# Kernel tuning notes

Measured on AMD Instinct MI355X. Metric: run time of the kernel, lower is better.

The kernel has to match this reference:

```python
import jax, jax.numpy as jnp
import numpy as np

B, S, D, H = 2, 2048, 1024, 16
DK = D // H

def setup_inputs() -> dict:
    key = jax.random.key(0)
    ks = jax.random.split(key, 12)
    s = 1.0 / np.sqrt(D)
    return {
        "q": jax.random.normal(ks[0], (B, S, D), jnp.float32),
        "k": jax.random.normal(ks[1], (B, S, D), jnp.float32),
        "v": jax.random.normal(ks[2], (B, S, D), jnp.float32),
        "mask": jnp.ones((1, 1, S, S), jnp.int32),
        "Wq": jax.random.normal(ks[3], (D, D), jnp.float32) * s,
        "bq": jnp.zeros((D,), jnp.float32),
        "Wk": jax.random.normal(ks[4], (D, D), jnp.float32) * s,
        "bk": jnp.zeros((D,), jnp.float32),
        "Wv": jax.random.normal(ks[5], (D, D), jnp.float32) * s,
        "bv": jnp.zeros((D,), jnp.float32),
        "Wo": jax.random.normal(ks[6], (D, D), jnp.float32) * s,
        "bo": jnp.zeros((D,), jnp.float32),
    }

def reference(q, k, v, mask, Wq, bq, Wk, bk, Wv, bv, Wo, bo):
    # projections (torch Linear: x @ W^T + b)
    Q = q @ Wq.T + bq
    K = k @ Wk.T + bk
    V = v @ Wv.T + bv
    # split heads: [B,S,D] -> [B,H,S,DK]
    def split(x):
        return x.reshape(B, S, H, DK).transpose(0, 2, 1, 3)
    Qh, Kh, Vh = split(Q), split(K), split(V)
    scores = jnp.einsum('bhqd,bhkd->bhqk', Qh, Kh) / jnp.sqrt(jnp.float32(DK))
    scores = jnp.where(mask == 0, jnp.float32(-1e9), scores)
    attn = jax.nn.softmax(scores, axis=-1)  # dropout p=0.0 -> identity
    x = jnp.einsum('bhqk,bhkd->bhqd', attn, Vh)
    x = x.transpose(0, 2, 1, 3).reshape(B, S, D)
    return x @ Wo.T + bo
```

## Files before the change

kernel.cpp:

```cpp
#include <hip/hip_runtime.h>
#include <hip/hip_bf16.h>
#include <stdint.h>

#define B_    2
#define S_    2048
#define D_    1024
#define H_    16
#define NTOK  (B_ * S_)

typedef __attribute__((ext_vector_type(8))) short bf16x8;
typedef __attribute__((ext_vector_type(4))) float f32x4;
typedef __attribute__((ext_vector_type(2))) float float2v;
typedef __attribute__((ext_vector_type(2))) __bf16 bfv2;

static __device__ __forceinline__ unsigned short f2bf(float f) {
    unsigned int u = __float_as_uint(f);
    unsigned int r = (u + 0x7FFFu + ((u >> 16) & 1u)) >> 16;
    return (unsigned short)r;
}
static __device__ __forceinline__ unsigned int pkbf(float a, float b) {
    float2v fv = {a, b};
    bfv2 r = __builtin_convertvector(fv, bfv2);
    unsigned int u;
    __builtin_memcpy(&u, &r, 4);
    return u;
}

using g_cu32 = __attribute__((address_space(1))) const unsigned int;
using l_u32  = __attribute__((address_space(3))) unsigned int;
static __device__ __forceinline__ void gld16(const void* g, void* l) {
    __builtin_amdgcn_global_load_lds((g_cu32*)g, (l_u32*)l, 16, 0, 0);
}

#define QN ((size_t)NTOK * D_)
#define WN ((size_t)D_ * D_)

__global__ __launch_bounds__(256) void prep_kernel(
    const float* __restrict__ q, const float* __restrict__ k, const float* __restrict__ v,
    const float* __restrict__ Wq, const float* __restrict__ Wk,
    const float* __restrict__ Wv, const float* __restrict__ Wo,
    const int* __restrict__ mask,
    unsigned short* __restrict__ qb, unsigned short* __restrict__ kb,
    unsigned short* __restrict__ vb, unsigned short* __restrict__ wqb,
    unsigned short* __restrict__ wkb, unsigned short* __restrict__ wvb,
    unsigned short* __restrict__ wob, int* __restrict__ flags) {
    __shared__ int anyz;
    if (blockIdx.x < 8192) {
        size_t i = ((size_t)blockIdx.x * 256 + threadIdx.x) * 8;
        const float* s; unsigned short* d; size_t off;
        if (i < QN)          { s = q; d = qb; off = i; }
        else if (i < 2 * QN) { s = k; d = kb; off = i - QN; }
        else if (i < 3 * QN) { s = v; d = vb; off = i - 2 * QN; }
        else {
            size_t j = i - 3 * QN;
            int wi = (int)(j >> 20);
            s = (wi == 0) ? Wq : (wi == 1) ? Wk : (wi == 2) ? Wv : Wo;
            d = (wi == 0) ? wqb : (wi == 1) ? wkb : (wi == 2) ? wvb : wob;
            off = j & (WN - 1);
        }
        float4 a = *(const float4*)(s + off);
        float4 b = *(const float4*)(s + off + 4);
        uint4 pk;
        pk.x = pkbf(a.x, a.y); pk.y = pkbf(a.z, a.w);
        pk.z = pkbf(b.x, b.y); pk.w = pkbf(b.z, b.w);
        *(uint4*)(d + off) = pk;
    } else {
        if (threadIdx.x == 0) anyz = 0;
        __syncthreads();
        int bid2 = blockIdx.x - 8192;
        const int qt = bid2 >> 5, kt = bid2 & 31;
        int az = 0;
        for (int i = threadIdx.x; i < 64 * 64; i += 256) {
            int r = i >> 6, c = i & 63;
            az |= (mask[(size_t)(qt * 64 + r) * S_ + kt * 64 + c] == 0) ? 1 : 0;
        }
        if (az) atomicOr(&anyz, 1);
        __syncthreads();
        if (threadIdx.x == 0) flags[qt * 32 + kt] = anyz;
    }
}

struct GemmArgs {
    const unsigned short* A[3];
    const unsigned short* W[3];
    const float* bias[3];
    void* C[3];
    int mode[3];
    float scale[3];
};

template<int BMT>
__global__ __launch_bounds__(256, 3) void gemm_async(GemmArgs ga) {
    constexpr int AG = BMT / 16;
    constexpr int MI = BMT / 32;
    const int z = blockIdx.z;
    const unsigned short* __restrict__ A = ga.A[z];
    const unsigned short* __restrict__ W = ga.W[z];
    const float* __restrict__ bias = ga.bias[z];
    void* C = ga.C[z];
    const int mode = ga.mode[z];
    const float scl = ga.scale[z];

    __shared__ unsigned short As[AG * 512];
    __shared__ unsigned short Bs[8 * 512];

    const int t    = threadIdx.x;
    const int lane = t & 63;
    const int w    = t >> 6;
    const int fr   = lane & 15;
    const int kq   = lane >> 4;
    const int wrow = w >> 1, wcol = w & 1;
    const int m0 = blockIdx.x * BMT, n0 = blockIdx.y * 128;

    const int sc = lane >> 4;
    const int sr = lane & 15;

    const unsigned short* ga0;
    const unsigned short* ga1 = nullptr;
    unsigned short* la0;
    unsigned short* la1 = nullptr;
    if constexpr (BMT == 128) {
        ga0 = A + (size_t)(m0 + (2 * w) * 16 + sr) * D_ + sc * 8;
        ga1 = ga0 + 16 * D_;
        la0 = &As[(2 * w) * 512];
        la1 = &As[(2 * w + 1) * 512];
    } else {
        ga0 = A + (size_t)(m0 + w * 16 + sr) * D_ + sc * 8;
        la0 = &As[w * 512];
    }
    const unsigned short* gw0 = W + (size_t)(n0 + (2 * w) * 16 + sr) * D_ + sc * 8;
    const unsigned short* gw1 = gw0 + 16 * D_;
    unsigned short* lw0 = &Bs[(2 * w) * 512];
    unsigned short* lw1 = &Bs[(2 * w + 1) * 512];

    int aOff[MI], bOff[4];
#pragma unroll
    for (int mi = 0; mi < MI; ++mi) aOff[mi] = (wrow * MI + mi) * 512 + (kq * 16 + fr) * 8;
#pragma unroll
    for (int ni = 0; ni < 4; ++ni) bOff[ni] = (wcol * 4 + ni) * 512 + (kq * 16 + fr) * 8;

    f32x4 acc[MI][4];
#pragma unroll
    for (int i = 0; i < MI; ++i)
#pragma unroll
        for (int j = 0; j < 4; ++j) acc[i][j] = (f32x4)0.0f;

    for (int k0 = 0; k0 < D_ / 32; ++k0) {
        gld16(ga0, la0);
        if constexpr (BMT == 128) gld16(ga1, la1);
        gld16(gw0, lw0);
        gld16(gw1, lw1);
        ga0 += 32; gw0 += 32; gw1 += 32;
        if constexpr (BMT == 128) ga1 += 32;
        __syncthreads();

        bf16x8 af[MI], bfr[4];
#pragma unroll
        for (int mi = 0; mi < MI; ++mi) af[mi] = *(const bf16x8*)&As[aOff[mi]];
#pragma unroll
        for (int ni = 0; ni < 4; ++ni) bfr[ni] = *(const bf16x8*)&Bs[bOff[ni]];
#pragma unroll
        for (int mi = 0; mi < MI; ++mi)
#pragma unroll
            for (int ni = 0; ni < 4; ++ni)
                acc[mi][ni] = __builtin_amdgcn_mfma_f32_16x16x32_bf16(
                    af[mi], bfr[ni], acc[mi][ni], 0, 0, 0);
        __syncthreads();
    }

    if (mode == 0) {
        float* Co = (float*)C;
#pragma unroll
        for (int ni = 0; ni < 4; ++ni) {
            int col = n0 + wcol * 64 + ni * 16 + fr;
            float bv = bias[col];
#pragma unroll
            for (int mi = 0; mi < MI; ++mi)
#pragma unroll
                for (int r = 0; r < 4; ++r) {
                    int row = m0 + wrow * (BMT / 2) + mi * 16 + kq * 4 + r;
                    Co[(size_t)row * D_ + col] = (acc[mi][ni][r] + bv) * scl;
                }
        }
    } else if (mode == 1) {
        unsigned short* Co = (unsigned short*)C;
#pragma unroll
        for (int ni = 0; ni < 4; ++ni) {
            int col = n0 + wcol * 64 + ni * 16 + fr;
            float bv = bias[col];
#pragma unroll
            for (int mi = 0; mi < MI; ++mi)
#pragma unroll
                for (int r = 0; r < 4; ++r) {
                    int row = m0 + wrow * (BMT / 2) + mi * 16 + kq * 4 + r;
                    Co[(size_t)row * D_ + col] = f2bf((acc[mi][ni][r] + bv) * scl);
                }
        }
    } else {
        unsigned short* Co = (unsigned short*)C;
#pragma unroll
        for (int ni = 0; ni < 4; ++ni) {
            int col = n0 + wcol * 64 + ni * 16 + fr;
            float bv = bias[col];
            int hh = col >> 6, d = col & 63;
#pragma unroll
            for (int mi = 0; mi < MI; ++mi) {
                int tok = m0 + wrow * (BMT / 2) + mi * 16 + kq * 4;
                int bb = tok >> 11, sbase = tok & (S_ - 1);
                uint2 pk;
                pk.x = pkbf((acc[mi][ni][0] + bv) * scl, (acc[mi][ni][1] + bv) * scl);
                pk.y = pkbf((acc[mi][ni][2] + bv) * scl, (acc[mi][ni][3] + bv) * scl);
                *(uint2*)(Co + ((size_t)((bb * H_ + hh) * 64 + d)) * S_ + sbase) = pk;
            }
        }
    }
}

__global__ __launch_bounds__(256, 4) void flash4(
    const unsigned short* __restrict__ Qb, const unsigned short* __restrict__ Kb,
    const unsigned short* __restrict__ Vtg, const int* __restrict__ mask,
    const int* __restrict__ flags, unsigned short* __restrict__ Xb) {
    __shared__ unsigned short Ks[2][4096];
    __shared__ unsigned short Vs[2][4096];
    __shared__ unsigned short Ps[4096];

    const int t    = threadIdx.x;
    const int lane = t & 63;
    const int w    = t >> 6;
    const int fr   = lane & 15;
    const int kq   = lane >> 4;
    const int qt = blockIdx.x, hd = blockIdx.y, b = blockIdx.z;
    const int q0 = qt * 64;
    const int swz = fr & 7;

    const unsigned short* qrow_p = Qb + (size_t)(b * S_ + q0 + w * 16 + fr) * D_ + hd * 64;
    bf16x8 qf[2];
    qf[0] = *(const bf16x8*)(qrow_p + kq * 8);
    qf[1] = *(const bf16x8*)(qrow_p + 32 + kq * 8);

    int fl = (lane < 32) ? flags[qt * 32 + lane] : 0;
    unsigned int fmask = (unsigned int)__ballot(fl != 0);

    const unsigned short* kbase =
        Kb + (size_t)(b * S_ + w * 16 + fr) * D_ + hd * 64 + kq * 8;
    const unsigned short* vbase =
        Vtg + ((size_t)((b * H_ + hd) * 64 + w * 16 + fr)) * S_ + kq * 8;

#pragma unroll
    for (int j = 0; j < 2; ++j) {
        gld16(kbase + j * 32, (char*)&Ks[0][0] + w * 2048 + j * 1024);
        gld16(vbase + j * 32, (char*)&Vs[0][0] + w * 2048 + j * 1024);
    }

    f32x4 o[4];
#pragma unroll
    for (int i = 0; i < 4; ++i) o[i] = (f32x4)0.0f;
    float l_i = 0.0f;

    for (int kt = 0; kt < 32; ++kt) {
        const int cur = kt & 1;
        __syncthreads();
        if (kt < 31) {
#pragma unroll
            for (int j = 0; j < 2; ++j) {
                gld16(kbase + (size_t)(kt + 1) * 64 * D_ + j * 32,
                      (char*)&Ks[cur ^ 1][0] + w * 2048 + j * 1024);
                gld16(vbase + (size_t)(kt + 1) * 64 + j * 32,
                      (char*)&Vs[cur ^ 1][0] + w * 2048 + j * 1024);
            }
        }

        f32x4 st[4];
#pragma unroll
        for (int mi = 0; mi < 4; ++mi) st[mi] = (f32x4)0.0f;
#pragma unroll
        for (int kk = 0; kk < 2; ++kk)
#pragma unroll
            for (int mi = 0; mi < 4; ++mi) {
                bf16x8 a = *(const bf16x8*)&Ks[cur][mi * 1024 + ((kk * 4 + kq) * 16 + fr) * 8];
                st[mi] = __builtin_amdgcn_mfma_f32_16x16x32_bf16(a, qf[kk], st[mi], 0, 0, 0);
            }

        if ((fmask >> kt) & 1u) {
#pragma unroll
            for (int mi = 0; mi < 4; ++mi) {
                int4 mv = *(const int4*)&mask[(size_t)(q0 + w * 16 + fr) * S_ + kt * 64 + mi * 16 + kq * 4];
                if (mv.x == 0) st[mi][0] = -3e8f;
                if (mv.y == 0) st[mi][1] = -3e8f;
                if (mv.z == 0) st[mi][2] = -3e8f;
                if (mv.w == 0) st[mi][3] = -3e8f;
            }
        }

#pragma unroll
        for (int mi = 0; mi < 4; ++mi) {
            float e0 = exp2f(st[mi][0]), e1 = exp2f(st[mi][1]);
            float e2 = exp2f(st[mi][2]), e3 = exp2f(st[mi][3]);
            l_i += (e0 + e1) + (e2 + e3);
            uint2 pk;
            pk.x = pkbf(e0, e1);
            pk.y = pkbf(e2, e3);
            int chunk = mi * 2 + (kq >> 1);
            *(uint2*)&Ps[(w * 16 + fr) * 64 + ((chunk ^ swz) << 3) + ((kq & 1) << 2)] = pk;
        }

#pragma unroll
        for (int kk = 0; kk < 2; ++kk) {
            int c = kk * 4 + kq;
            bf16x8 pb = *(const bf16x8*)&Ps[(w * 16 + fr) * 64 + ((c ^ swz) << 3)];
#pragma unroll
            for (int mi = 0; mi < 4; ++mi) {
                bf16x8 a = *(const bf16x8*)&Vs[cur][mi * 1024 + ((kk * 4 + kq) * 16 + fr) * 8];
                o[mi] = __builtin_amdgcn_mfma_f32_16x16x32_bf16(a, pb, o[mi], 0, 0, 0);
            }
        }
    }

    l_i += __shfl_xor(l_i, 16, 64);
    l_i += __shfl_xor(l_i, 32, 64);
    float rl = 1.0f / l_i;

#pragma unroll
    for (int mi = 0; mi < 4; ++mi) {
        uint2 pk;
        pk.x = pkbf(o[mi][0] * rl, o[mi][1] * rl);
        pk.y = pkbf(o[mi][2] * rl, o[mi][3] * rl);
        *(uint2*)(Xb + (size_t)(b * S_ + q0 + w * 16 + fr) * D_ + hd * 64 + mi * 16 + kq * 4) = pk;
    }
}

extern "C" void kernel_launch(void* const* d_in, const int* in_sizes, int n_in,
                              void* d_out, int out_size, void* d_ws, size_t ws_size,
                              hipStream_t stream) {
    const float* q    = (const float*)d_in[0];
    const float* k    = (const float*)d_in[1];
    const float* v    = (const float*)d_in[2];
    const int*   mask = (const int*)d_in[3];
    const float* Wq   = (const float*)d_in[4];
    const float* bq   = (const float*)d_in[5];
    const float* Wk   = (const float*)d_in[6];
    const float* bk   = (const float*)d_in[7];
    const float* Wv   = (const float*)d_in[8];
    const float* bv   = (const float*)d_in[9];
    const float* Wo   = (const float*)d_in[10];
    const float* bo   = (const float*)d_in[11];
    float* out = (float*)d_out;

    unsigned short* qb  = (unsigned short*)d_ws;
    unsigned short* kb  = qb + QN;
    unsigned short* vb  = kb + QN;
    unsigned short* Qf  = vb + QN;
    unsigned short* Kf  = Qf + QN;
    unsigned short* Vt  = Kf + QN;
    unsigned short* wqb = Vt + QN;
    unsigned short* wkb = wqb + WN;
    unsigned short* wvb = wkb + WN;
    unsigned short* wob = wvb + WN;
    int* flags = (int*)(wob + WN);

    const float SC = 0.18033688011112042f;

    prep_kernel<<<9216, 256, 0, stream>>>(q, k, v, Wq, Wk, Wv, Wo, mask,
                                          qb, kb, vb, wqb, wkb, wvb, wob, flags);

    GemmArgs g1;
    g1.A[0] = qb;  g1.W[0] = wqb; g1.bias[0] = bq; g1.C[0] = Qf; g1.mode[0] = 1; g1.scale[0] = SC;
    g1.A[1] = kb;  g1.W[1] = wkb; g1.bias[1] = bk; g1.C[1] = Kf; g1.mode[1] = 1; g1.scale[1] = 1.0f;
    g1.A[2] = vb;  g1.W[2] = wvb; g1.bias[2] = bv; g1.C[2] = Vt; g1.mode[2] = 2; g1.scale[2] = 1.0f;
    gemm_async<128><<<dim3(NTOK / 128, D_ / 128, 3), 256, 0, stream>>>(g1);

    flash4<<<dim3(S_ / 64, H_, B_), 256, 0, stream>>>(Qf, Kf, Vt, mask, flags, Qf);

    GemmArgs g2;
    g2.A[0] = Qf; g2.W[0] = wob; g2.bias[0] = bo; g2.C[0] = out; g2.mode[0] = 0; g2.scale[0] = 1.0f;
    g2.A[1] = g2.A[2] = nullptr; g2.W[1] = g2.W[2] = nullptr;
    g2.bias[1] = g2.bias[2] = nullptr; g2.C[1] = g2.C[2] = nullptr;
    g2.mode[1] = g2.mode[2] = 0; g2.scale[1] = g2.scale[2] = 1.0f;
    gemm_async<64><<<dim3(NTOK / 64, D_ / 128, 1), 256, 0, stream>>>(g2);
}
```

Before: 275.8 us.

## Double query rows per flash block and widen GEMM K-step to 64

```diff
diff --git a/kernel.cpp b/kernel.cpp
--- a/kernel.cpp
+++ b/kernel.cpp
@@ -91,8 +91,8 @@
 
 template<int BMT>
 __global__ __launch_bounds__(256, 3) void gemm_async(GemmArgs ga) {
-    constexpr int AG = BMT / 16;
     constexpr int MI = BMT / 32;
+    constexpr int AR = BMT / 32;
     const int z = blockIdx.z;
     const unsigned short* __restrict__ A = ga.A[z];
     const unsigned short* __restrict__ W = ga.W[z];
@@ -101,8 +101,8 @@
     const int mode = ga.mode[z];
     const float scl = ga.scale[z];
 
-    __shared__ unsigned short As[AG * 512];
-    __shared__ unsigned short Bs[8 * 512];
+    __shared__ unsigned short As[(BMT / 16) * 1024];
+    __shared__ unsigned short Ws[8 * 1024];
 
     const int t    = threadIdx.x;
     const int lane = t & 63;
@@ -115,29 +115,20 @@
     const int sc = lane >> 4;
     const int sr = lane & 15;
 
-    const unsigned short* ga0;
-    const unsigned short* ga1 = nullptr;
-    unsigned short* la0;
-    unsigned short* la1 = nullptr;
-    if constexpr (BMT == 128) {
-        ga0 = A + (size_t)(m0 + (2 * w) * 16 + sr) * D_ + sc * 8;
-        ga1 = ga0 + 16 * D_;
-        la0 = &As[(2 * w) * 512];
-        la1 = &As[(2 * w + 1) * 512];
-    } else {
-        ga0 = A + (size_t)(m0 + w * 16 + sr) * D_ + sc * 8;
-        la0 = &As[w * 512];
-    }
-    const unsigned short* gw0 = W + (size_t)(n0 + (2 * w) * 16 + sr) * D_ + sc * 8;
-    const unsigned short* gw1 = gw0 + 16 * D_;
-    unsigned short* lw0 = &Bs[(2 * w) * 512];
-    unsigned short* lw1 = &Bs[(2 * w + 1) * 512];
-
-    int aOff[MI], bOff[4];
-#pragma unroll
-    for (int mi = 0; mi < MI; ++mi) aOff[mi] = (wrow * MI + mi) * 512 + (kq * 16 + fr) * 8;
-#pragma unroll
-    for (int ni = 0; ni < 4; ++ni) bOff[ni] = (wcol * 4 + ni) * 512 + (kq * 16 + fr) * 8;
+    const unsigned short* gA[AR]; unsigned short* lA[AR];
+#pragma unroll
+    for (int i = 0; i < AR; ++i) {
+        int r = w * AR + i, rg = r >> 1, half = r & 1;
+        gA[i] = A + (size_t)(m0 + rg * 16 + sr) * D_ + half * 32 + sc * 8;
+        lA[i] = &As[r * 512];
+    }
+    const unsigned short* gW[4]; unsigned short* lW[4];
+#pragma unroll
+    for (int i = 0; i < 4; ++i) {
+        int r = w * 4 + i, rg = r >> 1, half = r & 1;
+        gW[i] = W + (size_t)(n0 + rg * 16 + sr) * D_ + half * 32 + sc * 8;
+        lW[i] = &Ws[r * 512];
+    }
 
     f32x4 acc[MI][4];
 #pragma unroll
@@ -145,26 +136,29 @@
 #pragma unroll
         for (int j = 0; j < 4; ++j) acc[i][j] = (f32x4)0.0f;
 
-    for (int k0 = 0; k0 < D_ / 32; ++k0) {
-        gld16(ga0, la0);
-        if constexpr (BMT == 128) gld16(ga1, la1);
-        gld16(gw0, lw0);
-        gld16(gw1, lw1);
-        ga0 += 32; gw0 += 32; gw1 += 32;
-        if constexpr (BMT == 128) ga1 += 32;
-        __syncthreads();
-
-        bf16x8 af[MI], bfr[4];
-#pragma unroll
-        for (int mi = 0; mi < MI; ++mi) af[mi] = *(const bf16x8*)&As[aOff[mi]];
-#pragma unroll
-        for (int ni = 0; ni < 4; ++ni) bfr[ni] = *(const bf16x8*)&Bs[bOff[ni]];
-#pragma unroll
-        for (int mi = 0; mi < MI; ++mi)
+    for (int k0 = 0; k0 < D_ / 64; ++k0) {
+#pragma unroll
+        for (int i = 0; i < AR; ++i) { gld16(gA[i], lA[i]); gA[i] += 64; }
+#pragma unroll
+        for (int i = 0; i < 4; ++i) { gld16(gW[i], lW[i]); gW[i] += 64; }
+        __syncthreads();
+
+#pragma unroll
+        for (int ks = 0; ks < 2; ++ks) {
+            bf16x8 af[MI], bfr[4];
+#pragma unroll
+            for (int mi = 0; mi < MI; ++mi)
+                af[mi] = *(const bf16x8*)&As[(wrow * MI + mi) * 1024 + ks * 512 + (kq * 16 + fr) * 8];
 #pragma unroll
             for (int ni = 0; ni < 4; ++ni)
-                acc[mi][ni] = __builtin_amdgcn_mfma_f32_16x16x32_bf16(
-                    af[mi], bfr[ni], acc[mi][ni], 0, 0, 0);
+                bfr[ni] = *(const bf16x8*)&Ws[(wcol * 4 + ni) * 1024 + ks * 512 + (kq * 16 + fr) * 8];
+#pragma unroll
+            for (int mi = 0; mi < MI; ++mi)
+#pragma unroll
+                for (int ni = 0; ni < 4; ++ni)
+                    acc[mi][ni] = __builtin_amdgcn_mfma_f32_16x16x32_bf16(
+                        af[mi], bfr[ni], acc[mi][ni], 0, 0, 0);
+        }
         __syncthreads();
     }
 
@@ -216,13 +210,13 @@
     }
 }
 
-__global__ __launch_bounds__(256, 4) void flash4(
+__global__ __launch_bounds__(256, 2) void flash5(
     const unsigned short* __restrict__ Qb, const unsigned short* __restrict__ Kb,
     const unsigned short* __restrict__ Vtg, const int* __restrict__ mask,
     const int* __restrict__ flags, unsigned short* __restrict__ Xb) {
     __shared__ unsigned short Ks[2][4096];
     __shared__ unsigned short Vs[2][4096];
-    __shared__ unsigned short Ps[4096];
+    __shared__ unsigned short Ps[8192];
 
     const int t    = threadIdx.x;
     const int lane = t & 63;
@@ -230,15 +224,19 @@
     const int fr   = lane & 15;
     const int kq   = lane >> 4;
     const int qt = blockIdx.x, hd = blockIdx.y, b = blockIdx.z;
-    const int q0 = qt * 64;
+    const int q0 = qt * 128;
+    const int qw = q0 + w * 32;
     const int swz = fr & 7;
 
-    const unsigned short* qrow_p = Qb + (size_t)(b * S_ + q0 + w * 16 + fr) * D_ + hd * 64;
-    bf16x8 qf[2];
-    qf[0] = *(const bf16x8*)(qrow_p + kq * 8);
-    qf[1] = *(const bf16x8*)(qrow_p + 32 + kq * 8);
-
-    int fl = (lane < 32) ? flags[qt * 32 + lane] : 0;
+    bf16x8 qf[2][2];
+#pragma unroll
+    for (int g = 0; g < 2; ++g) {
+        const unsigned short* qp = Qb + (size_t)(b * S_ + qw + g * 16 + fr) * D_ + hd * 64;
+        qf[g][0] = *(const bf16x8*)(qp + kq * 8);
+        qf[g][1] = *(const bf16x8*)(qp + 32 + kq * 8);
+    }
+
+    int fl = (lane < 32) ? flags[(qw >> 6) * 32 + lane] : 0;
     unsigned int fmask = (unsigned int)__ballot(fl != 0);
 
     const unsigned short* kbase =
@@ -252,10 +250,12 @@
         gld16(vbase + j * 32, (char*)&Vs[0][0] + w * 2048 + j * 1024);
     }
 
-    f32x4 o[4];
-#pragma unroll
-    for (int i = 0; i < 4; ++i) o[i] = (f32x4)0.0f;
-    float l_i = 0.0f;
+    f32x4 o[2][4];
+#pragma unroll
+    for (int g = 0; g < 2; ++g)
+#pragma unroll
+        for (int i = 0; i < 4; ++i) o[g][i] = (f32x4)0.0f;
+    float l_i[2] = {0.0f, 0.0f};
 
     for (int kt = 0; kt < 32; ++kt) {
         const int cur = kt & 1;
@@ -270,62 +270,74 @@
             }
         }
 
-        f32x4 st[4];
-#pragma unroll
-        for (int mi = 0; mi < 4; ++mi) st[mi] = (f32x4)0.0f;
+        f32x4 st[2][4];
+#pragma unroll
+        for (int g = 0; g < 2; ++g)
+#pragma unroll
+            for (int mi = 0; mi < 4; ++mi) st[g][mi] = (f32x4)0.0f;
 #pragma unroll
         for (int kk = 0; kk < 2; ++kk)
 #pragma unroll
             for (int mi = 0; mi < 4; ++mi) {
                 bf16x8 a = *(const bf16x8*)&Ks[cur][mi * 1024 + ((kk * 4 + kq) * 16 + fr) * 8];
-                st[mi] = __builtin_amdgcn_mfma_f32_16x16x32_bf16(a, qf[kk], st[mi], 0, 0, 0);
+                st[0][mi] = __builtin_amdgcn_mfma_f32_16x16x32_bf16(a, qf[0][kk], st[0][mi], 0, 0, 0);
+                st[1][mi] = __builtin_amdgcn_mfma_f32_16x16x32_bf16(a, qf[1][kk], st[1][mi], 0, 0, 0);
             }
 
         if ((fmask >> kt) & 1u) {
 #pragma unroll
+            for (int g = 0; g < 2; ++g)
+#pragma unroll
+                for (int mi = 0; mi < 4; ++mi) {
+                    int4 mv = *(const int4*)&mask[(size_t)(qw + g * 16 + fr) * S_ + kt * 64 + mi * 16 + kq * 4];
+                    if (mv.x == 0) st[g][mi][0] = -3e8f;
+                    if (mv.y == 0) st[g][mi][1] = -3e8f;
+                    if (mv.z == 0) st[g][mi][2] = -3e8f;
+                    if (mv.w == 0) st[g][mi][3] = -3e8f;
+                }
+        }
+
+#pragma unroll
+        for (int g = 0; g < 2; ++g)
+#pragma unroll
             for (int mi = 0; mi < 4; ++mi) {
-                int4 mv = *(const int4*)&mask[(size_t)(q0 + w * 16 + fr) * S_ + kt * 64 + mi * 16 + kq * 4];
-                if (mv.x == 0) st[mi][0] = -3e8f;
-                if (mv.y == 0) st[mi][1] = -3e8f;
-                if (mv.z == 0) st[mi][2] = -3e8f;
-                if (mv.w == 0) st[mi][3] = -3e8f;
-            }
-        }
-
-#pragma unroll
-        for (int mi = 0; mi < 4; ++mi) {
-            float e0 = exp2f(st[mi][0]), e1 = exp2f(st[mi][1]);
-            float e2 = exp2f(st[mi][2]), e3 = exp2f(st[mi][3]);
-            l_i += (e0 + e1) + (e2 + e3);
-            uint2 pk;
-            pk.x = pkbf(e0, e1);
-            pk.y = pkbf(e2, e3);
-            int chunk = mi * 2 + (kq >> 1);
-            *(uint2*)&Ps[(w * 16 + fr) * 64 + ((chunk ^ swz) << 3) + ((kq & 1) << 2)] = pk;
-        }
+                float e0 = exp2f(st[g][mi][0]), e1 = exp2f(st[g][mi][1]);
+                float e2 = exp2f(st[g][mi][2]), e3 = exp2f(st[g][mi][3]);
+                l_i[g] += (e0 + e1) + (e2 + e3);
+                uint2 pk;
+                pk.x = pkbf(e0, e1);
+                pk.y = pkbf(e2, e3);
+                int chunk = mi * 2 + (kq >> 1);
+                *(uint2*)&Ps[(w * 32 + g * 16 + fr) * 64 + ((chunk ^ swz) << 3) + ((kq & 1) << 2)] = pk;
+            }
 
 #pragma unroll
         for (int kk = 0; kk < 2; ++kk) {
             int c = kk * 4 + kq;
-            bf16x8 pb = *(const bf16x8*)&Ps[(w * 16 + fr) * 64 + ((c ^ swz) << 3)];
+            bf16x8 pb0 = *(const bf16x8*)&Ps[(w * 32 + fr) * 64 + ((c ^ swz) << 3)];
+            bf16x8 pb1 = *(const bf16x8*)&Ps[(w * 32 + 16 + fr) * 64 + ((c ^ swz) << 3)];
 #pragma unroll
             for (int mi = 0; mi < 4; ++mi) {
                 bf16x8 a = *(const bf16x8*)&Vs[cur][mi * 1024 + ((kk * 4 + kq) * 16 + fr) * 8];
-                o[mi] = __builtin_amdgcn_mfma_f32_16x16x32_bf16(a, pb, o[mi], 0, 0, 0);
-            }
-        }
-    }
-
-    l_i += __shfl_xor(l_i, 16, 64);
-    l_i += __shfl_xor(l_i, 32, 64);
-    float rl = 1.0f / l_i;
-
-#pragma unroll
-    for (int mi = 0; mi < 4; ++mi) {
-        uint2 pk;
-        pk.x = pkbf(o[mi][0] * rl, o[mi][1] * rl);
-        pk.y = pkbf(o[mi][2] * rl, o[mi][3] * rl);
-        *(uint2*)(Xb + (size_t)(b * S_ + q0 + w * 16 + fr) * D_ + hd * 64 + mi * 16 + kq * 4) = pk;
+                o[0][mi] = __builtin_amdgcn_mfma_f32_16x16x32_bf16(a, pb0, o[0][mi], 0, 0, 0);
+                o[1][mi] = __builtin_amdgcn_mfma_f32_16x16x32_bf16(a, pb1, o[1][mi], 0, 0, 0);
+            }
+        }
+    }
+
+#pragma unroll
+    for (int g = 0; g < 2; ++g) {
+        float lg = l_i[g];
+        lg += __shfl_xor(lg, 16, 64);
+        lg += __shfl_xor(lg, 32, 64);
+        float rl = 1.0f / lg;
+#pragma unroll
+        for (int mi = 0; mi < 4; ++mi) {
+            uint2 pk;
+            pk.x = pkbf(o[g][mi][0] * rl, o[g][mi][1] * rl);
+            pk.y = pkbf(o[g][mi][2] * rl, o[g][mi][3] * rl);
+            *(uint2*)(Xb + (size_t)(b * S_ + qw + g * 16 + fr) * D_ + hd * 64 + mi * 16 + kq * 4) = pk;
+        }
     }
 }
 
@@ -369,7 +381,7 @@
     g1.A[2] = vb;  g1.W[2] = wvb; g1.bias[2] = bv; g1.C[2] = Vt; g1.mode[2] = 2; g1.scale[2] = 1.0f;
     gemm_async<128><<<dim3(NTOK / 128, D_ / 128, 3), 256, 0, stream>>>(g1);
 
-    flash4<<<dim3(S_ / 64, H_, B_), 256, 0, stream>>>(Qf, Kf, Vt, mask, flags, Qf);
+    flash5<<<dim3(S_ / 128, H_, B_), 256, 0, stream>>>(Qf, Kf, Vt, mask, flags, Qf);
 
     GemmArgs g2;
     g2.A[0] = Qf; g2.W[0] = wob; g2.bias[0] = bo; g2.C[0] = out; g2.mode[0] = 0; g2.scale[0] = 1.0f;
```

Measured after the change: 277.8 us. About the same (+0.7%).
